# Kernel tuning notes

Hardware: AMD Instinct MI355X
Metric: run time of the kernel (lower is better)

The kernel has to match this reference:

```python
import jax, jax.numpy as jnp
import numpy as np

N_NEURON = 1024
N_PEPTIDE = 16
N_GENES = 1
BATCH = 2048
SQ = 32  # int(sqrt(N_NEURON))
DT = 1.0 / 120.0
STATE_SIZE = N_NEURON + N_GENES + N_NEURON + N_NEURON * N_PEPTIDE  # 18433


def setup_inputs() -> dict:
    key = jax.random.key(0)
    ks = jax.random.split(key, 10)
    # structured state: [ablate_mat | pc2 | neuron | peptide]
    ablate_mat = jnp.ones((BATCH, N_NEURON), jnp.float32)
    pc2 = jax.random.uniform(ks[0], (BATCH, N_GENES), jnp.float32)
    neuron = jax.random.normal(ks[1], (BATCH, N_NEURON), jnp.float32)
    peptide = jax.random.uniform(ks[2], (BATCH, N_NEURON * N_PEPTIDE), jnp.float32)
    state = jnp.concatenate([ablate_mat, pc2, neuron, peptide], axis=-1)
    u = jax.random.normal(ks[3], (BATCH, 1), jnp.float32)
    # uniform noise sample used by the exp firing noise; keep strictly < 1
    noise_u = jax.random.uniform(ks[4], (BATCH, N_NEURON), jnp.float32, 1e-6, 1.0 - 1e-6)
    D = jax.random.uniform(ks[5], (N_PEPTIDE,), jnp.float32)
    pep_prod_rate = jax.random.uniform(ks[6], (N_PEPTIDE,), jnp.float32)
    pep_decay_rate = jax.random.uniform(ks[7], (N_PEPTIDE,), jnp.float32)
    pep_action = jax.random.normal(ks[8], (N_PEPTIDE,), jnp.float32)
    synapse_matrix = jax.random.normal(ks[9], (N_NEURON, N_NEURON), jnp.float32) * 0.02
    neuron_decay = jnp.ones((1,), jnp.float32) * 0.5
    input_layer = jax.random.normal(jax.random.fold_in(key, 11), (N_NEURON,), jnp.float32)
    return dict(u=u, state=state, noise_u=noise_u, D=D, pep_prod_rate=pep_prod_rate,
                pep_decay_rate=pep_decay_rate, pep_action=pep_action,
                synapse_matrix=synapse_matrix, neuron_decay=neuron_decay,
                input_layer=input_layer)


def reference(u, state, noise_u, D, pep_prod_rate, pep_decay_rate, pep_action,
              synapse_matrix, neuron_decay, input_layer):
    # func = abs (log_train=False)
    Dp = jnp.abs(D)
    prod_r = jnp.abs(pep_prod_rate)
    decay_r = jnp.abs(pep_decay_rate)
    ndecay = jnp.abs(neuron_decay)

    # unpack state: [ablate | pc2 | neuron | peptide]
    ablate_mat = state[:, :N_NEURON]
    pc2 = state[:, N_NEURON:N_NEURON + N_GENES]
    neuron = state[:, N_NEURON + N_GENES:2 * N_NEURON + N_GENES]
    pep_flat = state[:, 2 * N_NEURON + N_GENES:]
    peptide = pep_flat.reshape(-1, N_NEURON, N_PEPTIDE)

    firing = jax.nn.relu(neuron) * ablate_mat
    neuron = neuron * ablate_mat

    # noisy_fire, noise='exp': firing = -(firing+0.01)*log(1-U)
    firing = -(firing + 0.01) * jnp.log1p(-noise_u)
    firing = jnp.clip(firing, 0.0, 10.0)

    # peptide production / decay
    pep_prod = prod_r * firing[:, :, None]           # (b, n, p)
    pep_decay = decay_r * peptide                    # (b, n, p)

    # wrap-around 2D Laplacian diffusion stencil on (SQ, SQ) grid
    ps = peptide.reshape(-1, SQ, SQ, N_PEPTIDE)
    lap = (jnp.roll(ps, -1, axis=1) + jnp.roll(ps, 1, axis=1)
           + jnp.roll(ps, -1, axis=2) + jnp.roll(ps, 1, axis=2) - 4.0 * ps)
    pep_diffuse = (Dp * lap).reshape(-1, N_NEURON, N_PEPTIDE)

    # neuron dynamics
    d_neuron = jnp.sum(peptide * pep_action, axis=-1) * pc2
    d_neuron = d_neuron + firing @ synapse_matrix
    d_neuron = d_neuron - neuron * ndecay
    d_neuron = d_neuron + input_layer * u            # (b,1)*(n,) broadcast

    d_peptide = (pep_prod - pep_decay + pep_diffuse).reshape(-1, N_NEURON * N_PEPTIDE)
    pep_new = pep_flat + d_peptide * DT
    neuron_new = (neuron + d_neuron * DT) * ablate_mat

    state_new = jnp.concatenate([ablate_mat, pc2, neuron_new, pep_new], axis=-1)
    # return_firing=True
    return firing, state_new
```

## Files before the change

### kernel.cpp

```cpp
#include <hip/hip_runtime.h>
#include <hip/hip_bf16.h>

#define N_NEURON 1024
#define N_PEPTIDE 16
#define N_GENES 1
#define BATCH 2048
#define SQ 32
#define DT_STEP (1.0f/120.0f)
#define S_STRIDE (N_NEURON + N_GENES + N_NEURON + N_NEURON*N_PEPTIDE)

typedef __attribute__((ext_vector_type(8))) short short8;
typedef __attribute__((ext_vector_type(4))) float floatx4;

__global__ __launch_bounds__(256) void synT_cast(const float* __restrict__ syn,
                                                 __hip_bfloat16* __restrict__ synT) {
    __shared__ float tile[32][33];
    const int n0 = blockIdx.x * 32;
    const int k0 = blockIdx.y * 32;
    const int tx = threadIdx.x & 31;
    const int ty = threadIdx.x >> 5;
    #pragma unroll
    for (int i = 0; i < 4; ++i)
        tile[ty + i*8][tx] = syn[(long)(k0 + ty + i*8) * N_NEURON + n0 + tx];
    __syncthreads();
    #pragma unroll
    for (int i = 0; i < 4; ++i)
        synT[(long)(n0 + ty + i*8) * N_NEURON + k0 + tx] =
            __float2bfloat16(tile[tx][ty + i*8]);
}

__global__ __launch_bounds__(256) void fused_elem(
    const float* __restrict__ u,
    const float* __restrict__ state,
    const float* __restrict__ noise,
    const float* __restrict__ D,
    const float* __restrict__ prod_g,
    const float* __restrict__ decay_g,
    const float* __restrict__ pact_g,
    const float* __restrict__ ndecay_g,
    const float* __restrict__ inL,
    float* __restrict__ firing_out,
    float* __restrict__ state_new,
    __hip_bfloat16* __restrict__ fbf)
{
    __shared__ float sf[N_NEURON];
    __shared__ float sn[N_NEURON];
    const int b = blockIdx.x;
    const int tid = threadIdx.x;
    const long bS = (long)b * S_STRIDE;
    const float u_b = u[b];
    const float pc2 = state[bS + N_NEURON];
    const float ndecay = fabsf(ndecay_g[0]);

    #pragma unroll
    for (int k = 0; k < 4; ++k) {
        const int n = tid + k * 256;
        const float ab = state[bS + n];
        const float nr = state[bS + N_NEURON + N_GENES + n];
        const float nm = nr * ab;
        float f = fmaxf(nr, 0.f) * ab;
        f = -(f + 0.01f) * log1pf(-noise[(long)b * N_NEURON + n]);
        f = fminf(fmaxf(f, 0.f), 10.f);
        firing_out[(long)b * N_NEURON + n] = f;
        fbf[(long)b * N_NEURON + n] = __float2bfloat16(f);
        state_new[bS + n] = ab;
        sf[n] = f;
        sn[n] = nm;
    }
    if (tid == 0) state_new[bS + N_NEURON] = pc2;
    __syncthreads();

    const int p = tid & 15;
    const float Dp      = fabsf(D[p]);
    const float prod_r  = fabsf(prod_g[p]);
    const float decay_r = fabsf(decay_g[p]);
    const float pact    = pact_g[p];
    const int g16 = tid >> 4;

    const float* __restrict__ pep = state + bS + 2 * N_NEURON + N_GENES;
    float* __restrict__ pep_new = state_new + bS + 2 * N_NEURON + N_GENES;

    for (int it = 0; it < 64; ++it) {
        const int n = it * 16 + g16;
        const int si = n >> 5, sj = n & 31;
        const int iup = ((((si + 31) & 31) * 32 + sj) << 4) + p;
        const int idn = ((((si + 1) & 31) * 32 + sj) << 4) + p;
        const int ilf = ((si * 32 + ((sj + 31) & 31)) << 4) + p;
        const int irt = ((si * 32 + ((sj + 1) & 31)) << 4) + p;
        const int idx = (n << 4) + p;
        const float c = pep[idx];
        const float lap = pep[iup] + pep[idn] + pep[ilf] + pep[irt] - 4.f * c;
        const float f = sf[n];
        pep_new[idx] = c + DT_STEP * (prod_r * f - decay_r * c + Dp * lap);

        float ps = c * pact;
        ps += __shfl_xor(ps, 1);
        ps += __shfl_xor(ps, 2);
        ps += __shfl_xor(ps, 4);
        ps += __shfl_xor(ps, 8);
        if (p == 0) {
            const float nm = sn[n];
            const float c0 = nm + DT_STEP * (ps * pc2 - nm * ndecay + inL[n] * u_b);
            state_new[bS + N_NEURON + N_GENES + n] = c0;
        }
    }
}

__global__ __launch_bounds__(256) void gemm_epi(
    const __hip_bfloat16* __restrict__ A,
    const __hip_bfloat16* __restrict__ BT,
    const float* __restrict__ state,
    float* __restrict__ state_new)
{
    const int tid = threadIdx.x;
    const int w = tid >> 6, lid = tid & 63;
    const int q = lid >> 4, l16 = lid & 15;
    const int m0 = blockIdx.x * 64 + (w & 1) * 32;
    const int n0 = blockIdx.y * 64 + (w >> 1) * 32;

    floatx4 acc[2][2] = {};
    for (int k0 = 0; k0 < 1024; k0 += 32) {
        short8 a[2], bfr[2];
        #pragma unroll
        for (int mi = 0; mi < 2; ++mi)
            a[mi] = *(const short8*)(A + (long)(m0 + mi * 16 + l16) * 1024 + k0 + q * 8);
        #pragma unroll
        for (int ni = 0; ni < 2; ++ni)
            bfr[ni] = *(const short8*)(BT + (long)(n0 + ni * 16 + l16) * 1024 + k0 + q * 8);
        #pragma unroll
        for (int mi = 0; mi < 2; ++mi)
            #pragma unroll
            for (int ni = 0; ni < 2; ++ni)
                acc[mi][ni] = __builtin_amdgcn_mfma_f32_16x16x32_bf16(
                    a[mi], bfr[ni], acc[mi][ni], 0, 0, 0);
    }

    #pragma unroll
    for (int mi = 0; mi < 2; ++mi)
    #pragma unroll
    for (int ni = 0; ni < 2; ++ni)
    #pragma unroll
    for (int r = 0; r < 4; ++r) {
        const int m = m0 + mi * 16 + q * 4 + r;
        const int n = n0 + ni * 16 + l16;
        const long sidx = (long)m * S_STRIDE;
        const float ab = state[sidx + n];
        const float c0 = state_new[sidx + N_NEURON + N_GENES + n];
        state_new[sidx + N_NEURON + N_GENES + n] = (c0 + DT_STEP * acc[mi][ni][r]) * ab;
    }
}

extern "C" void kernel_launch(void* const* d_in, const int* in_sizes, int n_in,
                              void* d_out, int out_size, void* d_ws, size_t ws_size,
                              hipStream_t stream) {
    const float* u      = (const float*)d_in[0];
    const float* state  = (const float*)d_in[1];
    const float* noise  = (const float*)d_in[2];
    const float* D      = (const float*)d_in[3];
    const float* prod   = (const float*)d_in[4];
    const float* decay  = (const float*)d_in[5];
    const float* pact   = (const float*)d_in[6];
    const float* syn    = (const float*)d_in[7];
    const float* ndec   = (const float*)d_in[8];
    const float* inL    = (const float*)d_in[9];

    float* firing = (float*)d_out;
    float* state_new = firing + (long)BATCH * N_NEURON;

    __hip_bfloat16* fbf  = (__hip_bfloat16*)d_ws;
    __hip_bfloat16* synT = fbf + (long)BATCH * N_NEURON;

    hipLaunchKernelGGL(synT_cast, dim3(32, 32), dim3(256), 0, stream, syn, synT);
    hipLaunchKernelGGL(fused_elem, dim3(BATCH), dim3(256), 0, stream,
                       u, state, noise, D, prod, decay, pact, ndec, inL,
                       firing, state_new, fbf);
    hipLaunchKernelGGL(gemm_epi, dim3(32, 16), dim3(256), 0, stream,
                       fbf, synT, state, state_new);
}
```

Measured before the change: 384.0 us.

## Split fused elementwise kernel into firing and peptide kernels, stage GEMM tiles in LDS

The per-batch fused kernel is split into a flat per-neuron firing kernel and a flat per-element peptide update kernel with an interleaved block mapping. This exposes far more parallelism than one block per batch row with a serial 64-iteration loop. log1pf is replaced by a hardware log2 approximation. The GEMM now stages A and B tiles through shared memory with a K step of 64. The cost is an extra launch, a firing round-trip through global memory, and a read-modify-write of the neuron slot. The fast log is also less accurate than log1p when noise is near zero.

```diff
diff --git a/kernel.cpp b/kernel.cpp
--- a/kernel.cpp
+++ b/kernel.cpp
@@ -8,6 +8,7 @@
 #define SQ 32
 #define DT_STEP (1.0f/120.0f)
 #define S_STRIDE (N_NEURON + N_GENES + N_NEURON + N_NEURON*N_PEPTIDE)
+#define LN2 0.6931471805599453f
 
 typedef __attribute__((ext_vector_type(8))) short short8;
 typedef __attribute__((ext_vector_type(4))) float floatx4;
@@ -29,110 +30,121 @@
             __float2bfloat16(tile[tx][ty + i*8]);
 }
 
-__global__ __launch_bounds__(256) void fused_elem(
+__global__ __launch_bounds__(256) void firing_stage(
     const float* __restrict__ u,
     const float* __restrict__ state,
     const float* __restrict__ noise,
-    const float* __restrict__ D,
-    const float* __restrict__ prod_g,
-    const float* __restrict__ decay_g,
-    const float* __restrict__ pact_g,
     const float* __restrict__ ndecay_g,
     const float* __restrict__ inL,
     float* __restrict__ firing_out,
     float* __restrict__ state_new,
     __hip_bfloat16* __restrict__ fbf)
 {
-    __shared__ float sf[N_NEURON];
-    __shared__ float sn[N_NEURON];
-    const int b = blockIdx.x;
-    const int tid = threadIdx.x;
+    const int idx = blockIdx.x * 256 + threadIdx.x;
+    const int b = idx >> 10, n = idx & 1023;
     const long bS = (long)b * S_STRIDE;
-    const float u_b = u[b];
-    const float pc2 = state[bS + N_NEURON];
+    const float ab = state[bS + n];
+    const float nr = state[bS + N_NEURON + N_GENES + n];
+    const float nm = nr * ab;
     const float ndecay = fabsf(ndecay_g[0]);
+    float f = fmaxf(nr, 0.f) * ab;
+    f = -(f + 0.01f) * (LN2 * __builtin_amdgcn_logf(1.0f - noise[idx]));
+    f = fminf(fmaxf(f, 0.f), 10.f);
+    firing_out[idx] = f;
+    fbf[idx] = __float2bfloat16(f);
+    state_new[bS + n] = ab;
+    state_new[bS + N_NEURON + N_GENES + n] =
+        nm + DT_STEP * (inL[n] * u[b] - nm * ndecay);
+    if (n == 0) state_new[bS + N_NEURON] = state[bS + N_NEURON];
+}
 
-    #pragma unroll
-    for (int k = 0; k < 4; ++k) {
-        const int n = tid + k * 256;
-        const float ab = state[bS + n];
-        const float nr = state[bS + N_NEURON + N_GENES + n];
-        const float nm = nr * ab;
-        float f = fmaxf(nr, 0.f) * ab;
-        f = -(f + 0.01f) * log1pf(-noise[(long)b * N_NEURON + n]);
-        f = fminf(fmaxf(f, 0.f), 10.f);
-        firing_out[(long)b * N_NEURON + n] = f;
-        fbf[(long)b * N_NEURON + n] = __float2bfloat16(f);
-        state_new[bS + n] = ab;
-        sf[n] = f;
-        sn[n] = nm;
-    }
-    if (tid == 0) state_new[bS + N_NEURON] = pc2;
-    __syncthreads();
+__global__ __launch_bounds__(256) void pep_update(
+    const float* __restrict__ state,
+    const float* __restrict__ firing_out,
+    const float* __restrict__ D,
+    const float* __restrict__ prod_g,
+    const float* __restrict__ decay_g,
+    const float* __restrict__ pact_g,
+    float* __restrict__ state_new)
+{
+    const int wid = (blockIdx.x & 7) * (131072 / 8) + (blockIdx.x >> 3);
+    const int e = wid * 256 + threadIdx.x;
+    const int b = e >> 14;
+    const int r = e & 16383;
+    const int n = r >> 4;
+    const int p = threadIdx.x & 15;
+    const long bS = (long)b * S_STRIDE;
+    const float* __restrict__ pep = state + bS + 2 * N_NEURON + N_GENES;
 
-    const int p = tid & 15;
-    const float Dp      = fabsf(D[p]);
-    const float prod_r  = fabsf(prod_g[p]);
-    const float decay_r = fabsf(decay_g[p]);
-    const float pact    = pact_g[p];
-    const int g16 = tid >> 4;
+    const int si = n >> 5, sj = n & 31;
+    const int iup = ((((si + 31) & 31) * 32 + sj) << 4) + p;
+    const int idn = ((((si +  1) & 31) * 32 + sj) << 4) + p;
+    const int ilf = ((si * 32 + ((sj + 31) & 31)) << 4) + p;
+    const int irt = ((si * 32 + ((sj +  1) & 31)) << 4) + p;
 
-    const float* __restrict__ pep = state + bS + 2 * N_NEURON + N_GENES;
-    float* __restrict__ pep_new = state_new + bS + 2 * N_NEURON + N_GENES;
+    const float c = pep[r];
+    const float lap = pep[iup] + pep[idn] + pep[ilf] + pep[irt] - 4.f * c;
+    const float f = firing_out[(b << 10) + n];
+    const float upd = c + DT_STEP * (fabsf(prod_g[p]) * f
+                                   - fabsf(decay_g[p]) * c
+                                   + fabsf(D[p]) * lap);
+    state_new[bS + 2 * N_NEURON + N_GENES + r] = upd;
 
-    for (int it = 0; it < 64; ++it) {
-        const int n = it * 16 + g16;
-        const int si = n >> 5, sj = n & 31;
-        const int iup = ((((si + 31) & 31) * 32 + sj) << 4) + p;
-        const int idn = ((((si + 1) & 31) * 32 + sj) << 4) + p;
-        const int ilf = ((si * 32 + ((sj + 31) & 31)) << 4) + p;
-        const int irt = ((si * 32 + ((sj + 1) & 31)) << 4) + p;
-        const int idx = (n << 4) + p;
-        const float c = pep[idx];
-        const float lap = pep[iup] + pep[idn] + pep[ilf] + pep[irt] - 4.f * c;
-        const float f = sf[n];
-        pep_new[idx] = c + DT_STEP * (prod_r * f - decay_r * c + Dp * lap);
-
-        float ps = c * pact;
-        ps += __shfl_xor(ps, 1);
-        ps += __shfl_xor(ps, 2);
-        ps += __shfl_xor(ps, 4);
-        ps += __shfl_xor(ps, 8);
-        if (p == 0) {
-            const float nm = sn[n];
-            const float c0 = nm + DT_STEP * (ps * pc2 - nm * ndecay + inL[n] * u_b);
-            state_new[bS + N_NEURON + N_GENES + n] = c0;
-        }
+    float ps = c * pact_g[p];
+    ps += __shfl_xor(ps, 1);
+    ps += __shfl_xor(ps, 2);
+    ps += __shfl_xor(ps, 4);
+    ps += __shfl_xor(ps, 8);
+    if (p == 0) {
+        const float pc2 = state[bS + N_NEURON];
+        float* dst = state_new + bS + N_NEURON + N_GENES + n;
+        *dst = *dst + DT_STEP * ps * pc2;
     }
 }
 
-__global__ __launch_bounds__(256) void gemm_epi(
+__global__ __launch_bounds__(256) void gemm_lds(
     const __hip_bfloat16* __restrict__ A,
     const __hip_bfloat16* __restrict__ BT,
     const float* __restrict__ state,
     float* __restrict__ state_new)
 {
+    __shared__ short As[64][72];
+    __shared__ short Bs[64][72];
     const int tid = threadIdx.x;
     const int w = tid >> 6, lid = tid & 63;
     const int q = lid >> 4, l16 = lid & 15;
-    const int m0 = blockIdx.x * 64 + (w & 1) * 32;
-    const int n0 = blockIdx.y * 64 + (w >> 1) * 32;
+    const int m0 = blockIdx.x * 64;
+    const int n0 = blockIdx.y * 64;
+    const int scol = (tid & 7) * 8;
 
     floatx4 acc[2][2] = {};
-    for (int k0 = 0; k0 < 1024; k0 += 32) {
-        short8 a[2], bfr[2];
+    for (int k0 = 0; k0 < 1024; k0 += 64) {
         #pragma unroll
-        for (int mi = 0; mi < 2; ++mi)
-            a[mi] = *(const short8*)(A + (long)(m0 + mi * 16 + l16) * 1024 + k0 + q * 8);
+        for (int rr = 0; rr < 2; ++rr) {
+            const int row = (tid >> 3) + rr * 32;
+            *(short8*)&As[row][scol] =
+                *(const short8*)(A + (long)(m0 + row) * 1024 + k0 + scol);
+            *(short8*)&Bs[row][scol] =
+                *(const short8*)(BT + (long)(n0 + row) * 1024 + k0 + scol);
+        }
+        __syncthreads();
         #pragma unroll
-        for (int ni = 0; ni < 2; ++ni)
-            bfr[ni] = *(const short8*)(BT + (long)(n0 + ni * 16 + l16) * 1024 + k0 + q * 8);
-        #pragma unroll
-        for (int mi = 0; mi < 2; ++mi)
+        for (int ks = 0; ks < 64; ks += 32) {
+            short8 a[2], bb[2];
+            #pragma unroll
+            for (int mi = 0; mi < 2; ++mi)
+                a[mi] = *(const short8*)&As[(w & 1) * 32 + mi * 16 + l16][ks + q * 8];
             #pragma unroll
             for (int ni = 0; ni < 2; ++ni)
-                acc[mi][ni] = __builtin_amdgcn_mfma_f32_16x16x32_bf16(
-                    a[mi], bfr[ni], acc[mi][ni], 0, 0, 0);
+                bb[ni] = *(const short8*)&Bs[(w >> 1) * 32 + ni * 16 + l16][ks + q * 8];
+            #pragma unroll
+            for (int mi = 0; mi < 2; ++mi)
+                #pragma unroll
+                for (int ni = 0; ni < 2; ++ni)
+                    acc[mi][ni] = __builtin_amdgcn_mfma_f32_16x16x32_bf16(
+                        a[mi], bb[ni], acc[mi][ni], 0, 0, 0);
+        }
+        __syncthreads();
     }
 
     #pragma unroll
@@ -140,13 +152,14 @@
     #pragma unroll
     for (int ni = 0; ni < 2; ++ni)
     #pragma unroll
-    for (int r = 0; r < 4; ++r) {
-        const int m = m0 + mi * 16 + q * 4 + r;
-        const int n = n0 + ni * 16 + l16;
+    for (int rr = 0; rr < 4; ++rr) {
+        const int m = m0 + (w & 1) * 32 + mi * 16 + q * 4 + rr;
+        const int n = n0 + (w >> 1) * 32 + ni * 16 + l16;
         const long sidx = (long)m * S_STRIDE;
         const float ab = state[sidx + n];
         const float c0 = state_new[sidx + N_NEURON + N_GENES + n];
-        state_new[sidx + N_NEURON + N_GENES + n] = (c0 + DT_STEP * acc[mi][ni][r]) * ab;
+        state_new[sidx + N_NEURON + N_GENES + n] =
+            (c0 + DT_STEP * acc[mi][ni][rr]) * ab;
     }
 }
 
@@ -171,9 +184,10 @@
     __hip_bfloat16* synT = fbf + (long)BATCH * N_NEURON;
 
     hipLaunchKernelGGL(synT_cast, dim3(32, 32), dim3(256), 0, stream, syn, synT);
-    hipLaunchKernelGGL(fused_elem, dim3(BATCH), dim3(256), 0, stream,
-                       u, state, noise, D, prod, decay, pact, ndec, inL,
-                       firing, state_new, fbf);
-    hipLaunchKernelGGL(gemm_epi, dim3(32, 16), dim3(256), 0, stream,
+    hipLaunchKernelGGL(firing_stage, dim3(BATCH * N_NEURON / 256), dim3(256), 0, stream,
+                       u, state, noise, ndec, inL, firing, state_new, fbf);
+    hipLaunchKernelGGL(pep_update, dim3(131072), dim3(256), 0, stream,
+                       state, firing, D, prod, decay, pact, state_new);
+    hipLaunchKernelGGL(gemm_lds, dim3(32, 16), dim3(256), 0, stream,
                        fbf, synT, state, state_new);
 }
```

Measured after the change: 416.6 us. 1.08x slower.
